# Kernel tuning notes

Measured on AMD Instinct MI355X. Metric: run time of the kernel, lower is better.

## Reference

```python
import jax, jax.numpy as jnp
import numpy as np

EMBED = 384
HEADS = 6
HEAD_SIZE = EMBED // HEADS
EPS = 1e-5


def _layernorm(x, g, b):
    mu = jnp.mean(x, axis=-1, keepdims=True)
    var = jnp.mean(jnp.square(x - mu), axis=-1, keepdims=True)
    return (x - mu) * jax.lax.rsqrt(var + EPS) * g + b


def setup_inputs() -> dict:
    key = jax.random.key(0)
    ks = jax.random.split(key, 16)
    B, T = 64, 256
    s_in = 1.0 / np.sqrt(EMBED)
    return {
        "x": jax.random.normal(ks[0], (B, T, EMBED), dtype=jnp.float32),
        # per-head q/k/v projections, stacked over heads: [H, C, D]
        "Wq": jax.random.normal(ks[1], (HEADS, EMBED, HEAD_SIZE), dtype=jnp.float32) * s_in,
        "bq": jnp.zeros((HEADS, HEAD_SIZE), dtype=jnp.float32),
        "Wk": jax.random.normal(ks[2], (HEADS, EMBED, HEAD_SIZE), dtype=jnp.float32) * s_in,
        "bk": jnp.zeros((HEADS, HEAD_SIZE), dtype=jnp.float32),
        "Wv": jax.random.normal(ks[3], (HEADS, EMBED, HEAD_SIZE), dtype=jnp.float32) * s_in,
        "bv": jnp.zeros((HEADS, HEAD_SIZE), dtype=jnp.float32),
        "Wp": jax.random.normal(ks[4], (EMBED, EMBED), dtype=jnp.float32) * s_in,
        "bp": jnp.zeros((EMBED,), dtype=jnp.float32),
        "W1": jax.random.normal(ks[5], (EMBED, EMBED), dtype=jnp.float32) * s_in,
        "b1": jnp.zeros((EMBED,), dtype=jnp.float32),
        "W2": jax.random.normal(ks[6], (EMBED, EMBED), dtype=jnp.float32) * s_in,
        "b2": jnp.zeros((EMBED,), dtype=jnp.float32),
        "ln1_g": jnp.ones((EMBED,), dtype=jnp.float32),
        "ln1_b": jnp.zeros((EMBED,), dtype=jnp.float32),
        "ln2_g": jnp.ones((EMBED,), dtype=jnp.float32),
        "ln2_b": jnp.zeros((EMBED,), dtype=jnp.float32),
    }


def reference(x, Wq, bq, Wk, bk, Wv, bv, Wp, bp, W1, b1, W2, b2,
              ln1_g, ln1_b, ln2_g, ln2_b):
    B, T, C = x.shape
    h = _layernorm(x, ln1_g, ln1_b)
    # batched per-head projections: [B,H,T,D]
    q = jnp.einsum('btc,hcd->bhtd', h, Wq) + bq[None, :, None, :]
    k = jnp.einsum('btc,hcd->bhtd', h, Wk) + bk[None, :, None, :]
    v = jnp.einsum('btc,hcd->bhtd', h, Wv) + bv[None, :, None, :]
    # NOTE: original scales by embed_size**0.5 (C=384), not head_size.
    wei = jnp.einsum('bhtd,bhsd->bhts', q, k) / jnp.sqrt(jnp.float32(C))
    causal = jnp.tril(jnp.ones((T, T), dtype=bool))
    wei = jnp.where(causal[None, None], wei, -jnp.inf)
    wei = jax.nn.softmax(wei, axis=-1)  # dropout = identity in eval
    attn = jnp.einsum('bhts,bhsd->bhtd', wei, v)  # [B,H,T,D]
    # concat heads in head order -> [B,T,C]
    attn = attn.transpose(0, 2, 1, 3).reshape(B, T, C)
    x = x + attn @ Wp + bp
    h2 = _layernorm(x, ln2_g, ln2_b)
    ff = jax.nn.relu(h2 @ W1 + b1) @ W2 + b2
    return x + ff
```

## Files before the change

kernel.cpp:

```cpp
#include <hip/hip_runtime.h>

typedef _Float16 f16;
typedef _Float16 half8 __attribute__((ext_vector_type(8)));
typedef _Float16 half4v __attribute__((ext_vector_type(4)));
typedef float floatx4 __attribute__((ext_vector_type(4)));

#define B_ 64
#define T_ 256
#define C_ 384
#define H_ 6
#define D_ 64
#define NROWS (B_*T_)

typedef __attribute__((address_space(3))) void lds_void_t;
typedef const __attribute__((address_space(1))) void gvoid_t;

__device__ __forceinline__ void g2lds16(const void* g, void* l) {
  __builtin_amdgcn_global_load_lds((gvoid_t*)g, (lds_void_t*)l, 16, 0, 0);
}

__global__ __launch_bounds__(256) void prep_ln_kernel(
    const float* __restrict__ Wq, const float* __restrict__ Wk, const float* __restrict__ Wv,
    const float* __restrict__ bq, const float* __restrict__ bk, const float* __restrict__ bv,
    const float* __restrict__ Wp, const float* __restrict__ W1, const float* __restrict__ W2,
    f16* __restrict__ Wqkv_t, f16* __restrict__ Wp_t, f16* __restrict__ W1_t, f16* __restrict__ W2_t,
    float* __restrict__ bqkv,
    const float* __restrict__ x, const float* __restrict__ gamma, const float* __restrict__ beta,
    f16* __restrict__ hout)
{
  const int bid = blockIdx.x;
  const int tid = threadIdx.x;
  if (bid >= 217) {
    int row = (bid - 217) * 4 + (tid >> 6);
    int lane = tid & 63;
    const float* xr = x + (size_t)row * 384;
    float v[6]; float s = 0.f;
#pragma unroll
    for (int j = 0; j < 6; j++) { v[j] = xr[lane + 64*j]; s += v[j]; }
#pragma unroll
    for (int m = 1; m < 64; m <<= 1) s += __shfl_xor(s, m);
    float mu = s * (1.f/384.f);
    float var = 0.f;
#pragma unroll
    for (int j = 0; j < 6; j++) { float d = v[j]-mu; var += d*d; }
#pragma unroll
    for (int m = 1; m < 64; m <<= 1) var += __shfl_xor(var, m);
    float rs = rsqrtf(var * (1.f/384.f) + 1e-5f);
    f16* orow = hout + (size_t)row*384;
#pragma unroll
    for (int j = 0; j < 6; j++) {
      int col = lane + 64*j;
      orow[col] = (f16)((v[j]-mu)*rs*gamma[col] + beta[col]);
    }
    return;
  }
  if (bid == 216) {
    for (int i = tid; i < 1152; i += 256) {
      float v;
      if (i < 384)      v = bq[i];
      else if (i < 768) v = bk[i - 384];
      else              v = bv[i - 768];
      bqkv[i] = v;
    }
    return;
  }
  __shared__ __align__(16) float tile[64*68];
  const float* src; int srcStride; f16* dst;
  if (bid < 108) {
    int mat = bid / 36, rem = bid - mat*36;
    int h = rem / 6, kt = rem - h*6;
    const float* W = (mat == 0) ? Wq : (mat == 1) ? Wk : Wv;
    src = W + (size_t)(h*384 + kt*64)*64;
    srcStride = 64;
    dst = Wqkv_t + (size_t)(mat*384 + h*64)*384 + kt*64;
  } else {
    int b2 = bid - 108;
    int mat = b2 / 36, rem = b2 - mat*36;
    int kt = rem / 6, ct = rem - kt*6;
    const float* W = (mat == 0) ? Wp : (mat == 1) ? W1 : W2;
    src = W + (size_t)(kt*64)*384 + ct*64;
    srcStride = 384;
    f16* O = (mat == 0) ? Wp_t : (mat == 1) ? W1_t : W2_t;
    dst = O + (size_t)(ct*64)*384 + kt*64;
  }
#pragma unroll
  for (int i = 0; i < 4; i++) {
    int idx = i*256 + tid;
    int r = idx >> 4, c4 = idx & 15;
    float4 v = *(const float4*)(src + (size_t)r*srcStride + c4*4);
    *(float4*)(&tile[r*68 + c4*4]) = v;
  }
  __syncthreads();
#pragma unroll
  for (int i = 0; i < 4; i++) {
    int idx = i*256 + tid;
    int d = idx >> 4, k4 = idx & 15;
    half4v o;
#pragma unroll
    for (int j = 0; j < 4; j++) o[j] = (f16)tile[(k4*4 + j)*68 + d];
    *(half4v*)(dst + (size_t)d*384 + k4*4) = o;
  }
}

__global__ __launch_bounds__(256) void ln_kernel(const float* __restrict__ x,
    const float* __restrict__ gamma, const float* __restrict__ beta, f16* __restrict__ out)
{
  int row = blockIdx.x * 4 + (threadIdx.x >> 6);
  int lane = threadIdx.x & 63;
  const float* xr = x + (size_t)row * 384;
  float v[6]; float s = 0.f;
#pragma unroll
  for (int j = 0; j < 6; j++) { v[j] = xr[lane + 64*j]; s += v[j]; }
#pragma unroll
  for (int m = 1; m < 64; m <<= 1) s += __shfl_xor(s, m);
  float mu = s * (1.f/384.f);
  float var = 0.f;
#pragma unroll
  for (int j = 0; j < 6; j++) { float d = v[j]-mu; var += d*d; }
#pragma unroll
  for (int m = 1; m < 64; m <<= 1) var += __shfl_xor(var, m);
  float rs = rsqrtf(var * (1.f/384.f) + 1e-5f);
  f16* orow = out + (size_t)row*384;
#pragma unroll
  for (int j = 0; j < 6; j++) {
    int col = lane + 64*j;
    orow[col] = (f16)((v[j]-mu)*rs*gamma[col] + beta[col]);
  }
}

template<int MODE>
__global__ __launch_bounds__(256) void gemm_kernel(
    const f16* __restrict__ A, const f16* __restrict__ Bt,
    const float* __restrict__ bias, const float* __restrict__ res,
    void* __restrict__ outp, int ldo)
{
  __shared__ __align__(16) f16 As[2][128*32];
  __shared__ __align__(16) f16 Bs[2][128*32];
  const int tid = threadIdx.x;
  const int lane = tid & 63, w = tid >> 6;
  const int wm = w >> 1, wn = w & 1;
  const int q = lane >> 4, c15 = lane & 15;
  const long row0 = (long)blockIdx.x * 128;
  const long col0 = (long)blockIdx.y * 128;
  floatx4 acc[4][4] = {};

  const int c0 = tid,        r0c = c0 >> 2, p0 = c0 & 3, g0 = p0 ^ ((r0c >> 1) & 3);
  const int c1 = 256 + tid,  r1c = c1 >> 2, p1 = c1 & 3, g1 = p1 ^ ((r1c >> 1) & 3);
  const f16* Arow0 = A  + (row0 + r0c)*384 + g0*8;
  const f16* Arow1 = A  + (row0 + r1c)*384 + g1*8;
  const f16* Brow0 = Bt + (col0 + r0c)*384 + g0*8;
  const f16* Brow1 = Bt + (col0 + r1c)*384 + g1*8;
  const int dof0 = (w*64)*8, dof1 = (256 + w*64)*8;

  for (int k0 = 0; k0 < 384; k0 += 64) {
#pragma unroll
    for (int hf = 0; hf < 2; hf++) {
      int kk = k0 + hf*32;
      g2lds16(Arow0 + kk, &As[hf][dof0]);
      g2lds16(Arow1 + kk, &As[hf][dof1]);
      g2lds16(Brow0 + kk, &Bs[hf][dof0]);
      g2lds16(Brow1 + kk, &Bs[hf][dof1]);
    }
    __syncthreads();
#pragma unroll
    for (int hf = 0; hf < 2; hf++) {
      half8 af[4], bf[4];
#pragma unroll
      for (int mi = 0; mi < 4; mi++) {
        int r = wm*64 + mi*16 + c15;
        int ph = q ^ ((r >> 1) & 3);
        af[mi] = *(const half8*)(&As[hf][r*32 + ph*8]);
      }
#pragma unroll
      for (int ni = 0; ni < 4; ni++) {
        int r = wn*64 + ni*16 + c15;
        int ph = q ^ ((r >> 1) & 3);
        bf[ni] = *(const half8*)(&Bs[hf][r*32 + ph*8]);
      }
#pragma unroll
      for (int mi = 0; mi < 4; mi++)
#pragma unroll
        for (int ni = 0; ni < 4; ni++)
          acc[mi][ni] = __builtin_amdgcn_mfma_f32_16x16x32_f16(af[mi], bf[ni], acc[mi][ni], 0, 0, 0);
    }
    __syncthreads();
  }

#pragma unroll
  for (int ni = 0; ni < 4; ni++) {
    long col = col0 + wn*64 + ni*16 + c15;
    float bv = bias[col];
#pragma unroll
    for (int mi = 0; mi < 4; mi++) {
      long rowb = row0 + wm*64 + mi*16 + q*4;
#pragma unroll
      for (int r = 0; r < 4; r++) {
        float vo = acc[mi][ni][r] + bv;
        if (MODE == 1) vo = vo > 0.f ? vo : 0.f;
        long o = (rowb + r) * (long)ldo + col;
        if (MODE == 2) {
          ((float*)outp)[o] = vo + res[o];
        } else {
          ((f16*)outp)[o] = (f16)vo;
        }
      }
    }
  }
}

__global__ __launch_bounds__(512, 2) void attn_kernel(const f16* __restrict__ qkv,
                                                      f16* __restrict__ attn_out)
{
  __shared__ __align__(16) char kvbuf[32768];
  __shared__ __align__(16) f16 Pbuf[8][16*64];
  f16* Ks = (f16*)kvbuf;
  unsigned int* vTw = (unsigned int*)kvbuf;
  f16* vT = (f16*)kvbuf;

  const int tid = threadIdx.x;
  const int bid = blockIdx.x;
  const int bh = bid >> 1, qt2 = bid & 1;
  const int b = bh / 6, h = bh - b*6;
  const f16* qp = qkv + (size_t)b*256*1152 + h*64;
  const f16* kp = qp + 384;
  const f16* vp = qp + 768;
  const int lane = tid & 63, w = tid >> 6;
  const int q = lane >> 4, c15 = lane & 15;

  {
    const int iters = (qt2 + 1) * 2;
    for (int i = 0; i < iters; i++) {
      int pc = i*512 + tid;
      int rc = pc >> 3, p = pc & 7;
      int c = p ^ (rc & 7);
      g2lds16(kp + (size_t)rc*1152 + c*8, (char*)kvbuf + (size_t)(i*512 + w*64)*16);
    }
  }

  const int nmax = qt2*8 + w;
  const int trow0 = qt2*128 + w*16;
  const f16* qrow = qp + (size_t)(trow0 + c15)*1152 + q*8;
  half8 aq0 = *(const half8*)(qrow);
  half8 aq1 = *(const half8*)(qrow + 32);

  __syncthreads();

  floatx4 sacc[16];
  __builtin_amdgcn_s_setprio(1);
#pragma unroll
  for (int ni = 0; ni < 16; ni++) {
    if (ni <= nmax) {
      int s = ni*16 + c15;
      const f16* kr = Ks + s*64;
      int p0 = q ^ (s & 7);
      half8 b0 = *(const half8*)(kr + p0*8);
      half8 b1 = *(const half8*)(kr + (p0 ^ 4)*8);
      floatx4 a = {0.f, 0.f, 0.f, 0.f};
      a = __builtin_amdgcn_mfma_f32_16x16x32_f16(aq0, b0, a, 0, 0, 0);
      a = __builtin_amdgcn_mfma_f32_16x16x32_f16(aq1, b1, a, 0, 0, 0);
      sacc[ni] = a;
    }
  }
  __builtin_amdgcn_s_setprio(0);
  __syncthreads();

  half8 va[2], vb[2];
#pragma unroll
  for (int i = 0; i < 2; i++) {
    if (i <= qt2) {
      int idx = i*512 + tid;
      int sp = idx >> 3, part = idx & 7;
      const f16* v0 = vp + (size_t)(2*sp)*1152 + part*8;
      va[i] = *(const half8*)(v0);
      vb[i] = *(const half8*)(v0 + 1152);
    }
  }

  const float scale = 0.051031036307982884f;
  float mx[4] = {-1e30f, -1e30f, -1e30f, -1e30f};
#pragma unroll
  for (int ni = 0; ni < 16; ni++) {
    if (ni < nmax) {
#pragma unroll
      for (int r = 0; r < 4; r++) { float v = sacc[ni][r]*scale; sacc[ni][r] = v; mx[r] = fmaxf(mx[r], v); }
    } else if (ni == nmax) {
#pragma unroll
      for (int r = 0; r < 4; r++) {
        float v = sacc[ni][r]*scale;
        v = (c15 <= q*4 + r) ? v : -1e30f;
        sacc[ni][r] = v; mx[r] = fmaxf(mx[r], v);
      }
    }
  }
#pragma unroll
  for (int r = 0; r < 4; r++) {
    mx[r] = fmaxf(mx[r], __shfl_xor(mx[r], 1));
    mx[r] = fmaxf(mx[r], __shfl_xor(mx[r], 2));
    mx[r] = fmaxf(mx[r], __shfl_xor(mx[r], 4));
    mx[r] = fmaxf(mx[r], __shfl_xor(mx[r], 8));
  }
  float l[4] = {0.f, 0.f, 0.f, 0.f};
#pragma unroll
  for (int ni = 0; ni < 16; ni++) {
    if (ni <= nmax) {
#pragma unroll
      for (int r = 0; r < 4; r++) { float p = __expf(sacc[ni][r] - mx[r]); sacc[ni][r] = p; l[r] += p; }
    }
  }
#pragma unroll
  for (int r = 0; r < 4; r++) {
    l[r] += __shfl_xor(l[r], 1);
    l[r] += __shfl_xor(l[r], 2);
    l[r] += __shfl_xor(l[r], 4);
    l[r] += __shfl_xor(l[r], 8);
  }

#pragma unroll
  for (int i = 0; i < 2; i++) {
    if (i <= qt2) {
      int idx = i*512 + tid;
      int sp = idx >> 3, part = idx & 7;
      int csp = sp >> 2, spw = sp & 3;
#pragma unroll
      for (int j = 0; j < 8; j++) {
        int d = part*8 + j;
        int swz = (d & 15) ^ (d >> 3);
        int p = csp ^ swz;
        union { struct { f16 lo, hi; } s; unsigned int u; } pk;
        pk.s.lo = va[i][j]; pk.s.hi = vb[i][j];
        vTw[d*128 + p*4 + spw] = pk.u;
      }
    }
  }
  __syncthreads();

  f16* Pw = &Pbuf[w][0];
  floatx4 oacc[4] = {};
  const int kend_w = (nmax + 1) * 16;
#pragma unroll
  for (int ch = 0; ch < 4; ch++) {
    if (ch*64 < kend_w) {
#pragma unroll
      for (int nl = 0; nl < 4; nl++) {
        int ni = ch*4 + nl;
        if (ni <= nmax) {
#pragma unroll
          for (int r = 0; r < 4; r++) {
            int row = q*4 + r;
            int colp = nl*16 + c15;
            int php = (colp >> 3) ^ (row & 7);
            Pw[row*64 + php*8 + (colp & 7)] = (f16)sacc[ni][r];
          }
        } else if (ni == nmax + 1) {
#pragma unroll
          for (int r = 0; r < 4; r++) {
            int row = q*4 + r;
            int colp = nl*16 + c15;
            int php = (colp >> 3) ^ (row & 7);
            Pw[row*64 + php*8 + (colp & 7)] = (f16)0.f;
          }
        }
      }
      __builtin_amdgcn_s_setprio(1);
#pragma unroll
      for (int kc = 0; kc < 2; kc++) {
        if (ch*64 + kc*32 < kend_w) {
          int pc = (kc*4 + q) ^ (c15 & 7);
          half8 ap = *(const half8*)(Pw + c15*64 + pc*8);
          int sc = ch*8 + kc*4 + q;
#pragma unroll
          for (int nt = 0; nt < 4; nt++) {
            int d = nt*16 + c15;
            int swz = (d & 15) ^ (d >> 3);
            half8 bv = *(const half8*)(vT + d*256 + ((sc ^ swz))*8);
            oacc[nt] = __builtin_amdgcn_mfma_f32_16x16x32_f16(ap, bv, oacc[nt], 0, 0, 0);
          }
        }
      }
      __builtin_amdgcn_s_setprio(0);
    }
  }

  float rl[4];
#pragma unroll
  for (int r = 0; r < 4; r++) rl[r] = 1.0f / l[r];
#pragma unroll
  for (int nt = 0; nt < 4; nt++) {
#pragma unroll
    for (int r = 0; r < 4; r++) {
      int t = trow0 + q*4 + r;
      int d = nt*16 + c15;
      attn_out[(size_t)(b*256 + t)*384 + h*64 + d] = (f16)(oacc[nt][r] * rl[r]);
    }
  }
}

extern "C" void kernel_launch(void* const* d_in, const int* in_sizes, int n_in,
                              void* d_out, int out_size, void* d_ws, size_t ws_size,
                              hipStream_t stream) {
  const float* x   = (const float*)d_in[0];
  const float* Wq  = (const float*)d_in[1];
  const float* bq  = (const float*)d_in[2];
  const float* Wk  = (const float*)d_in[3];
  const float* bk  = (const float*)d_in[4];
  const float* Wv  = (const float*)d_in[5];
  const float* bv  = (const float*)d_in[6];
  const float* Wp  = (const float*)d_in[7];
  const float* bp  = (const float*)d_in[8];
  const float* W1  = (const float*)d_in[9];
  const float* b1  = (const float*)d_in[10];
  const float* W2  = (const float*)d_in[11];
  const float* b2  = (const float*)d_in[12];
  const float* g1  = (const float*)d_in[13];
  const float* be1 = (const float*)d_in[14];
  const float* g2  = (const float*)d_in[15];
  const float* be2 = (const float*)d_in[16];

  char* ws = (char*)d_ws;
  size_t off = 0;
  auto alloc = [&](size_t bytes) -> void* {
    void* p = ws + off;
    off += (bytes + 255) & ~(size_t)255;
    return p;
  };
  f16*   Wqkv_t = (f16*)  alloc(1152*384*sizeof(f16));
  f16*   Wp_t   = (f16*)  alloc(384*384*sizeof(f16));
  f16*   W1_t   = (f16*)  alloc(384*384*sizeof(f16));
  f16*   W2_t   = (f16*)  alloc(384*384*sizeof(f16));
  float* bqkv   = (float*)alloc(1152*sizeof(float));
  f16*   h      = (f16*)  alloc((size_t)NROWS*384*sizeof(f16));
  f16*   qkv    = (f16*)  alloc((size_t)NROWS*1152*sizeof(f16));
  f16*   attnb  = (f16*)  alloc((size_t)NROWS*384*sizeof(f16));
  float* x2     = (float*)alloc((size_t)NROWS*384*sizeof(float));
  f16*   h2     = (f16*)  alloc((size_t)NROWS*384*sizeof(f16));
  f16*   mid    = (f16*)  alloc((size_t)NROWS*384*sizeof(f16));

  prep_ln_kernel<<<217 + NROWS/4, 256, 0, stream>>>(Wq, Wk, Wv, bq, bk, bv, Wp, W1, W2,
                                                    Wqkv_t, Wp_t, W1_t, W2_t, bqkv,
                                                    x, g1, be1, h);
  gemm_kernel<0><<<dim3(128, 9), 256, 0, stream>>>(h, Wqkv_t, bqkv, nullptr, qkv, 1152);
  attn_kernel<<<B_*H_*2, 512, 0, stream>>>(qkv, attnb);
  gemm_kernel<2><<<dim3(128, 3), 256, 0, stream>>>(attnb, Wp_t, bp, x, x2, 384);
  ln_kernel<<<NROWS/4, 256, 0, stream>>>(x2, g2, be2, h2);
  gemm_kernel<1><<<dim3(128, 3), 256, 0, stream>>>(h2, W1_t, b1, nullptr, mid, 384);
  gemm_kernel<2><<<dim3(128, 3), 256, 0, stream>>>(mid, W2_t, b2, x2, (float*)d_out, 384);
}
```

Measured before the change: 199.6 us.

## Fuse projection, residual, LayerNorm and MLP into one row-block tail kernel

Replaces the four tail launches (output projection GEMM, LayerNorm, FFN up GEMM, FFN down GEMM) with a single kernel. Each 512-thread block owns 64 full rows, so the LayerNorm reduction runs in-block. The h2 and mid activations stay in LDS as swizzled f16 tiles and the residual is kept in registers. This removes the x2, h2 and mid global round-trips and three launches. In exchange it uses large LDS per block, has only 256 blocks, and computes variance as E[x^2]-mu^2.

Result: faster. 189.7 us (-5.0%).

```diff
diff --git a/kernel.cpp b/kernel.cpp
--- a/kernel.cpp
+++ b/kernel.cpp
@@ -102,37 +102,9 @@
   }
 }
 
-__global__ __launch_bounds__(256) void ln_kernel(const float* __restrict__ x,
-    const float* __restrict__ gamma, const float* __restrict__ beta, f16* __restrict__ out)
-{
-  int row = blockIdx.x * 4 + (threadIdx.x >> 6);
-  int lane = threadIdx.x & 63;
-  const float* xr = x + (size_t)row * 384;
-  float v[6]; float s = 0.f;
-#pragma unroll
-  for (int j = 0; j < 6; j++) { v[j] = xr[lane + 64*j]; s += v[j]; }
-#pragma unroll
-  for (int m = 1; m < 64; m <<= 1) s += __shfl_xor(s, m);
-  float mu = s * (1.f/384.f);
-  float var = 0.f;
-#pragma unroll
-  for (int j = 0; j < 6; j++) { float d = v[j]-mu; var += d*d; }
-#pragma unroll
-  for (int m = 1; m < 64; m <<= 1) var += __shfl_xor(var, m);
-  float rs = rsqrtf(var * (1.f/384.f) + 1e-5f);
-  f16* orow = out + (size_t)row*384;
-#pragma unroll
-  for (int j = 0; j < 6; j++) {
-    int col = lane + 64*j;
-    orow[col] = (f16)((v[j]-mu)*rs*gamma[col] + beta[col]);
-  }
-}
-
-template<int MODE>
-__global__ __launch_bounds__(256) void gemm_kernel(
+__global__ __launch_bounds__(256) void gemm_qkv_kernel(
     const f16* __restrict__ A, const f16* __restrict__ Bt,
-    const float* __restrict__ bias, const float* __restrict__ res,
-    void* __restrict__ outp, int ldo)
+    const float* __restrict__ bias, f16* __restrict__ outp, int ldo)
 {
   __shared__ __align__(16) f16 As[2][128*32];
   __shared__ __align__(16) f16 Bs[2][128*32];
@@ -196,13 +168,7 @@
 #pragma unroll
       for (int r = 0; r < 4; r++) {
         float vo = acc[mi][ni][r] + bv;
-        if (MODE == 1) vo = vo > 0.f ? vo : 0.f;
-        long o = (rowb + r) * (long)ldo + col;
-        if (MODE == 2) {
-          ((float*)outp)[o] = vo + res[o];
-        } else {
-          ((f16*)outp)[o] = (f16)vo;
-        }
+        outp[(rowb + r) * (long)ldo + col] = (f16)vo;
       }
     }
   }
@@ -393,6 +359,234 @@
       attn_out[(size_t)(b*256 + t)*384 + h*64 + d] = (f16)(oacc[nt][r] * rl[r]);
     }
   }
+}
+
+__global__ __launch_bounds__(512, 2) void tail_kernel(
+    const f16* __restrict__ A, const f16* __restrict__ WpT,
+    const f16* __restrict__ W1T, const f16* __restrict__ W2T,
+    const float* __restrict__ bp, const float* __restrict__ b1, const float* __restrict__ b2,
+    const float* __restrict__ x, const float* __restrict__ g2, const float* __restrict__ be2,
+    float* __restrict__ out)
+{
+  __shared__ __align__(16) f16 As[2][64*32];
+  __shared__ __align__(16) f16 Bs[2][384*32];
+  __shared__ __align__(16) f16 h2b[12][64*32];
+  __shared__ __align__(16) f16 midb[12][64*32];
+  __shared__ float lnred[2][64][4];
+  __shared__ float lnmv[2][64];
+
+  const int tid = threadIdx.x;
+  const int lane = tid & 63, w = tid >> 6;
+  const int wm = w >> 2, wn = w & 3;
+  const int q = lane >> 4, c15 = lane & 15;
+  const long row0 = (long)blockIdx.x * 64;
+
+  const int cA = w*64 + lane;
+  const int rA = cA >> 2, pA_ = cA & 3, gA = pA_ ^ ((rA >> 1) & 3);
+  const f16* srcA = A + (row0 + rA)*384 + gA*8;
+  auto boff = [&](int cb) -> long {
+    int rc = cb >> 2, p = cb & 3, g = p ^ ((rc >> 1) & 3);
+    return (long)rc*384 + g*8;
+  };
+  const long offBa0 = boff((w >= 4 ? (w-4) : 0)*64 + lane);
+  const long offBa1 = boff(256 + w*64 + lane);
+  const long offBa2 = boff(768 + w*64 + lane);
+  const long offBa3 = boff(1280 + (w < 4 ? w : 0)*64 + lane);
+  const long offBp0 = boff(w*64 + lane);
+  const long offBp1 = boff(512 + w*64 + lane);
+  const long offBp2 = boff(1024 + w*64 + lane);
+
+  floatx4 acc[2][6] = {};
+
+#define T_STAGE_A(buf, kk) do { \
+    if (w < 4) { \
+      g2lds16(srcA + (kk), &As[buf][(w*64)*8]); \
+      g2lds16(WpT + offBa3 + (kk), &Bs[buf][(1280 + w*64)*8]); \
+    } else { \
+      g2lds16(WpT + offBa0 + (kk), &Bs[buf][((w-4)*64)*8]); \
+    } \
+    g2lds16(WpT + offBa1 + (kk), &Bs[buf][(256 + w*64)*8]); \
+    g2lds16(WpT + offBa2 + (kk), &Bs[buf][(768 + w*64)*8]); \
+  } while (0)
+
+#define T_STAGE_B(buf, kk, BT) do { \
+    g2lds16(BT + offBp0 + (kk), &Bs[buf][(w*64)*8]); \
+    g2lds16(BT + offBp1 + (kk), &Bs[buf][(512 + w*64)*8]); \
+    g2lds16(BT + offBp2 + (kk), &Bs[buf][(1024 + w*64)*8]); \
+  } while (0)
+
+#define T_COMP(ABUF_EXPR, buf) do { \
+    half8 af[2], bf[6]; \
+    _Pragma("unroll") \
+    for (int mi = 0; mi < 2; mi++) { \
+      int r = wm*32 + mi*16 + c15; \
+      int ph = q ^ ((r >> 1) & 3); \
+      af[mi] = *(const half8*)(&(ABUF_EXPR)[r*32 + ph*8]); \
+    } \
+    _Pragma("unroll") \
+    for (int ni = 0; ni < 6; ni++) { \
+      int rb = wn*96 + ni*16 + c15; \
+      int phb = q ^ ((rb >> 1) & 3); \
+      bf[ni] = *(const half8*)(&Bs[buf][rb*32 + phb*8]); \
+    } \
+    _Pragma("unroll") \
+    for (int mi = 0; mi < 2; mi++) \
+      _Pragma("unroll") \
+      for (int ni = 0; ni < 6; ni++) \
+        acc[mi][ni] = __builtin_amdgcn_mfma_f32_16x16x32_f16(af[mi], bf[ni], acc[mi][ni], 0, 0, 0); \
+  } while (0)
+
+  T_STAGE_A(0, 0);
+  __syncthreads();
+#pragma unroll
+  for (int t = 0; t < 11; ++t) {
+    T_STAGE_A((t + 1) & 1, (t + 1) * 32);
+    T_COMP(As[t & 1], t & 1);
+    __syncthreads();
+  }
+  T_COMP(As[1], 1);
+
+  float vals[2][6][4];
+  {
+    float colb[6], cg[6], cb2[6];
+#pragma unroll
+    for (int ni = 0; ni < 6; ni++) {
+      int col = wn*96 + ni*16 + c15;
+      colb[ni] = bp[col]; cg[ni] = g2[col]; cb2[ni] = be2[col];
+    }
+#pragma unroll
+    for (int mi = 0; mi < 2; mi++) {
+#pragma unroll
+      for (int rr = 0; rr < 4; rr++) {
+        long row = row0 + wm*32 + mi*16 + q*4 + rr;
+#pragma unroll
+        for (int ni = 0; ni < 6; ni++) {
+          int col = wn*96 + ni*16 + c15;
+          float v = acc[mi][ni][rr] + colb[ni] + x[row*384 + col];
+          vals[mi][ni][rr] = v;
+        }
+      }
+    }
+#pragma unroll
+    for (int mi = 0; mi < 2; mi++) {
+#pragma unroll
+      for (int rr = 0; rr < 4; rr++) {
+        float s = 0.f, s2 = 0.f;
+#pragma unroll
+        for (int ni = 0; ni < 6; ni++) { float v = vals[mi][ni][rr]; s += v; s2 += v*v; }
+        s  += __shfl_xor(s, 1);  s  += __shfl_xor(s, 2);  s  += __shfl_xor(s, 4);  s  += __shfl_xor(s, 8);
+        s2 += __shfl_xor(s2, 1); s2 += __shfl_xor(s2, 2); s2 += __shfl_xor(s2, 4); s2 += __shfl_xor(s2, 8);
+        if (c15 == 0) {
+          int lr = wm*32 + mi*16 + q*4 + rr;
+          lnred[0][lr][wn] = s;
+          lnred[1][lr][wn] = s2;
+        }
+      }
+    }
+    __syncthreads();
+    if (tid < 64) {
+      float s = 0.f, s2 = 0.f;
+#pragma unroll
+      for (int j = 0; j < 4; j++) { s += lnred[0][tid][j]; s2 += lnred[1][tid][j]; }
+      float mu = s * (1.f/384.f);
+      float var = s2 * (1.f/384.f) - mu*mu;
+      lnmv[0][tid] = mu;
+      lnmv[1][tid] = rsqrtf(var + 1e-5f);
+    }
+    __syncthreads();
+#pragma unroll
+    for (int mi = 0; mi < 2; mi++) {
+#pragma unroll
+      for (int rr = 0; rr < 4; rr++) {
+        int lr = wm*32 + mi*16 + q*4 + rr;
+        float mu = lnmv[0][lr], rs = lnmv[1][lr];
+        int s_ = (lr >> 1) & 3;
+#pragma unroll
+        for (int ni = 0; ni < 6; ni++) {
+          int cc = wn*96 + ni*16 + c15;
+          float hv = (vals[mi][ni][rr] - mu)*rs*cg[ni] + cb2[ni];
+          int chunk = cc >> 5, kk2 = cc & 31;
+          int pos = ((kk2 >> 3) ^ s_)*8 + (kk2 & 7);
+          h2b[chunk][lr*32 + pos] = (f16)hv;
+        }
+      }
+    }
+  }
+  T_STAGE_B(0, 0, W1T);
+  __syncthreads();
+
+#pragma unroll
+  for (int mi = 0; mi < 2; mi++)
+#pragma unroll
+    for (int ni = 0; ni < 6; ni++)
+      acc[mi][ni] = floatx4{0.f, 0.f, 0.f, 0.f};
+#pragma unroll
+  for (int t = 0; t < 11; ++t) {
+    T_STAGE_B((t + 1) & 1, (t + 1) * 32, W1T);
+    T_COMP(h2b[t], t & 1);
+    __syncthreads();
+  }
+  T_COMP(h2b[11], 1);
+
+  {
+    float colb[6];
+#pragma unroll
+    for (int ni = 0; ni < 6; ni++) colb[ni] = b1[wn*96 + ni*16 + c15];
+#pragma unroll
+    for (int mi = 0; mi < 2; mi++) {
+#pragma unroll
+      for (int rr = 0; rr < 4; rr++) {
+        int lr = wm*32 + mi*16 + q*4 + rr;
+        int s_ = (lr >> 1) & 3;
+#pragma unroll
+        for (int ni = 0; ni < 6; ni++) {
+          int cc = wn*96 + ni*16 + c15;
+          float v = acc[mi][ni][rr] + colb[ni];
+          v = v > 0.f ? v : 0.f;
+          int chunk = cc >> 5, kk2 = cc & 31;
+          int pos = ((kk2 >> 3) ^ s_)*8 + (kk2 & 7);
+          midb[chunk][lr*32 + pos] = (f16)v;
+        }
+      }
+    }
+  }
+  T_STAGE_B(0, 0, W2T);
+  __syncthreads();
+
+#pragma unroll
+  for (int mi = 0; mi < 2; mi++)
+#pragma unroll
+    for (int ni = 0; ni < 6; ni++)
+      acc[mi][ni] = floatx4{0.f, 0.f, 0.f, 0.f};
+#pragma unroll
+  for (int t = 0; t < 11; ++t) {
+    T_STAGE_B((t + 1) & 1, (t + 1) * 32, W2T);
+    T_COMP(midb[t], t & 1);
+    __syncthreads();
+  }
+  T_COMP(midb[11], 1);
+
+  {
+    float colb[6];
+#pragma unroll
+    for (int ni = 0; ni < 6; ni++) colb[ni] = b2[wn*96 + ni*16 + c15];
+#pragma unroll
+    for (int mi = 0; mi < 2; mi++) {
+#pragma unroll
+      for (int rr = 0; rr < 4; rr++) {
+        long row = row0 + wm*32 + mi*16 + q*4 + rr;
+#pragma unroll
+        for (int ni = 0; ni < 6; ni++) {
+          int col = wn*96 + ni*16 + c15;
+          out[row*384 + col] = acc[mi][ni][rr] + colb[ni] + vals[mi][ni][rr];
+        }
+      }
+    }
+  }
+
+#undef T_STAGE_A
+#undef T_STAGE_B
+#undef T_COMP
 }
 
 extern "C" void kernel_launch(void* const* d_in, const int* in_sizes, int n_in,
@@ -431,17 +625,12 @@
   f16*   h      = (f16*)  alloc((size_t)NROWS*384*sizeof(f16));
   f16*   qkv    = (f16*)  alloc((size_t)NROWS*1152*sizeof(f16));
   f16*   attnb  = (f16*)  alloc((size_t)NROWS*384*sizeof(f16));
-  float* x2     = (float*)alloc((size_t)NROWS*384*sizeof(float));
-  f16*   h2     = (f16*)  alloc((size_t)NROWS*384*sizeof(f16));
-  f16*   mid    = (f16*)  alloc((size_t)NROWS*384*sizeof(f16));
 
   prep_ln_kernel<<<217 + NROWS/4, 256, 0, stream>>>(Wq, Wk, Wv, bq, bk, bv, Wp, W1, W2,
                                                     Wqkv_t, Wp_t, W1_t, W2_t, bqkv,
                                                     x, g1, be1, h);
-  gemm_kernel<0><<<dim3(128, 9), 256, 0, stream>>>(h, Wqkv_t, bqkv, nullptr, qkv, 1152);
+  gemm_qkv_kernel<<<dim3(128, 9), 256, 0, stream>>>(h, Wqkv_t, bqkv, qkv, 1152);
   attn_kernel<<<B_*H_*2, 512, 0, stream>>>(qkv, attnb);
-  gemm_kernel<2><<<dim3(128, 3), 256, 0, stream>>>(attnb, Wp_t, bp, x, x2, 384);
-  ln_kernel<<<NROWS/4, 256, 0, stream>>>(x2, g2, be2, h2);
-  gemm_kernel<1><<<dim3(128, 3), 256, 0, stream>>>(h2, W1_t, b1, nullptr, mid, 384);
-  gemm_kernel<2><<<dim3(128, 3), 256, 0, stream>>>(mid, W2_t, b2, x2, (float*)d_out, 384);
+  tail_kernel<<<NROWS/64, 512, 0, stream>>>(attnb, Wp_t, W1_t, W2_t, bp, b1, b2,
+                                            x, g2, be2, (float*)d_out);
 }
```
